# Kernel tuning notes

Hardware: AMD Instinct MI355X
Metric: run time of the kernel (lower is better)

Reference implementation:

```python
import jax, jax.numpy as jnp
import numpy as np

B, N, F = 1048576, 20, 7
RADIUS = 0.15
L1, L2 = 0.1, 2.0


def setup_inputs() -> dict:
    key = jax.random.key(0)
    ks = jax.random.split(key, 8)
    half = N // 2
    return {
        "x": jax.random.normal(ks[0], (B, N, F), dtype=jnp.float32),
        "W1": jax.random.normal(ks[1], (39, 64), dtype=jnp.float32) * 0.1,
        "b1": jax.random.normal(ks[2], (64,), dtype=jnp.float32) * 0.1,
        "W2": jax.random.normal(ks[3], (64, 64), dtype=jnp.float32) * 0.1,
        "b2": jax.random.normal(ks[4], (64,), dtype=jnp.float32) * 0.1,
        "W3": jax.random.normal(ks[5], (64, 5), dtype=jnp.float32) * 0.1,
        "b3": jax.random.normal(ks[6], (5,), dtype=jnp.float32) * 0.1,
        "idx": jax.random.randint(ks[7], (8,), 0, half, dtype=jnp.int32),
    }


def _build_observation(x, idx):
    # x: [B, N, 7]; agent_index = 0 (init kwarg)
    agent_index = 0
    half = N // 2
    Bsz = x.shape[0]
    pos = x[:, agent_index, 0:2]                      # [B,2]
    o_self = x[:, agent_index, 0:5]                   # [B,5]

    # three random agent neighbors: rel goal-like quantity, then a zero column
    xi = x[:, idx[0:3], :]                            # [B,3,7]
    rel = xi[..., 5:7] + xi[..., 0:2] - pos[:, None]  # [B,3,2]
    mid = jnp.concatenate(
        [rel, jnp.zeros((Bsz, 3, 1), dtype=x.dtype)], axis=2
    ).reshape(Bsz, 9)

    # five random obstacles (second half): distance-masked relative pos + features
    jdx = idx[3:8] + half
    xo = x[:, jdx, :]                                 # [B,5,7]
    d = xo[..., 0:2] - pos[:, None]                   # [B,5,2]
    dist = jnp.linalg.norm(d, axis=-1)                # [B,5]
    mask = (dist < RADIUS)[..., None]                 # [B,5,1]
    a = jnp.where(mask, d, 0.0)                       # [B,5,2]
    f = jnp.where(mask, xo[..., 2:5], 0.0)            # [B,5,3]
    obst = jnp.concatenate([a, f], axis=2).reshape(Bsz, 25)

    return jnp.concatenate([o_self, mid, obst], axis=1)  # [B,39]


def reference(x, W1, b1, W2, b2, W3, b3, idx):
    obs = _build_observation(x, idx)
    h = jax.nn.relu(obs @ W1 + b1)
    h = jax.nn.relu(h @ W2 + b2)
    r = h @ W3 + b3                                   # [B,5]
    res = jnp.stack([r[:, 1] - r[:, 2], r[:, 3] - r[:, 4]], axis=1) * L1
    res = jnp.where(jnp.abs(res) > 1.0, jnp.sign(res) * L2, res)
    return res
```

## Files before the change

### kernel.cpp

```cpp
#include <hip/hip_runtime.h>
#include <math.h>


#define NROW 20
#define NF   7
#define ITEM_F (NROW * NF)
#define BLOCK 256

typedef float v2 __attribute__((ext_vector_type(2)));

__device__ __forceinline__ void row_fma(v2 (&h)[32], float o,
                                        const float* __restrict__ wrow) {
    const v2* w = (const v2*)wrow;
    #pragma unroll
    for (int k = 0; k < 32; k++) {
        v2 ov; ov.x = o; ov.y = o;
        h[k] = __builtin_elementwise_fma(ov, w[k], h[k]);
    }
}

__global__ __launch_bounds__(BLOCK, 2) void maddpg_kernel(
    const float* __restrict__ x,
    const float* __restrict__ W1, const float* __restrict__ b1,
    const float* __restrict__ W2, const float* __restrict__ b2,
    const float* __restrict__ W3, const float* __restrict__ b3,
    const int*   __restrict__ idx,
    float2*      __restrict__ out,
    int nitems)
{
    const int tid = threadIdx.x;
    const long b  = (long)blockIdx.x * BLOCK + tid;
    if (b >= nitems) return;

    const float* xb = x + b * (long)ITEM_F;

    float4 s0 = *(const float4*)(xb);
    float  s4 = xb[4];
    const float px = s0.x, py = s0.y;

    float mo[6];
    #pragma unroll
    for (int t = 0; t < 3; t++) {
        const float* xr = xb + idx[t] * NF;
        float2 p01 = *(const float2*)(xr);
        float2 p56 = *(const float2*)(xr + 5);
        mo[2*t + 0] = p56.x + p01.x - px;
        mo[2*t + 1] = p56.y + p01.y - py;
    }

    float oa[5][5];
    int   anyt[5];
    #pragma unroll
    for (int t = 0; t < 5; t++) {
        const float* xr = xb + (idx[3 + t] + NROW/2) * NF;
        float4 q  = *(const float4*)(xr);
        float  q4 = xr[4];
        float dx = q.x - px, dy = q.y - py;
        bool  m  = sqrtf(dx*dx + dy*dy) < 0.15f;
        oa[t][0] = m ? dx  : 0.0f;
        oa[t][1] = m ? dy  : 0.0f;
        oa[t][2] = m ? q.z : 0.0f;
        oa[t][3] = m ? q.w : 0.0f;
        oa[t][4] = m ? q4  : 0.0f;
        anyt[t]  = __any(m);
    }

    v2 h[32];
    const v2* b1v = (const v2*)b1;
    #pragma unroll
    for (int k = 0; k < 32; k++) h[k] = b1v[k];

    row_fma(h, s0.x, W1 + 0*64);
    row_fma(h, s0.y, W1 + 1*64);
    row_fma(h, s0.z, W1 + 2*64);
    row_fma(h, s0.w, W1 + 3*64);
    row_fma(h, s4,   W1 + 4*64);
    #pragma unroll
    for (int t = 0; t < 3; t++) {
        row_fma(h, mo[2*t + 0], W1 + (5 + 3*t)*64);
        row_fma(h, mo[2*t + 1], W1 + (6 + 3*t)*64);
    }
    #pragma unroll
    for (int t = 0; t < 5; t++) {
        if (anyt[t]) {
            #pragma unroll
            for (int j = 0; j < 5; j++)
                row_fma(h, oa[t][j], W1 + (14 + 5*t + j)*64);
        }
    }

    v2 a[32];
    #pragma unroll
    for (int k = 0; k < 32; k++) {
        a[k].x = fmaxf(h[k].x, 0.0f);
        a[k].y = fmaxf(h[k].y, 0.0f);
    }

    const v2* b2v = (const v2*)b2;
    #pragma unroll
    for (int k = 0; k < 32; k++) h[k] = b2v[k];
    #pragma unroll
    for (int i = 0; i < 64; i++) {
        float o = (i & 1) ? a[i >> 1].y : a[i >> 1].x;
        row_fma(h, o, W2 + i*64);
    }
    #pragma unroll
    for (int k = 0; k < 32; k++) {
        a[k].x = fmaxf(h[k].x, 0.0f);
        a[k].y = fmaxf(h[k].y, 0.0f);
    }

    v2 rA; rA.x = b3[1]; rA.y = b3[2];
    v2 rB; rB.x = b3[3]; rB.y = b3[4];
    #pragma unroll
    for (int i = 0; i < 64; i++) {
        float o = (i & 1) ? a[i >> 1].y : a[i >> 1].x;
        const float* w = W3 + i*5;
        v2 ov; ov.x = o; ov.y = o;
        v2 wA; wA.x = w[1]; wA.y = w[2];
        v2 wB; wB.x = w[3]; wB.y = w[4];
        rA = __builtin_elementwise_fma(ov, wA, rA);
        rB = __builtin_elementwise_fma(ov, wB, rB);
    }

    float v0 = (rA.x - rA.y) * 0.1f;
    float v1 = (rB.x - rB.y) * 0.1f;
    if (fabsf(v0) > 1.0f) v0 = copysignf(2.0f, v0);
    if (fabsf(v1) > 1.0f) v1 = copysignf(2.0f, v1);

    out[b] = make_float2(v0, v1);
}

extern "C" void kernel_launch(void* const* d_in, const int* in_sizes, int n_in,
                              void* d_out, int out_size, void* d_ws, size_t ws_size,
                              hipStream_t stream) {
    const float* x  = (const float*)d_in[0];
    const float* W1 = (const float*)d_in[1];
    const float* b1 = (const float*)d_in[2];
    const float* W2 = (const float*)d_in[3];
    const float* b2 = (const float*)d_in[4];
    const float* W3 = (const float*)d_in[5];
    const float* b3 = (const float*)d_in[6];
    const int*   idx = (const int*)d_in[7];
    float2* out = (float2*)d_out;

    int nitems = in_sizes[0] / ITEM_F;
    int grid = (nitems + BLOCK - 1) / BLOCK;
    maddpg_kernel<<<grid, BLOCK, 0, stream>>>(x, W1, b1, W2, b2, W3, b3, idx,
                                              out, nitems);
}
```

Baseline: 935.0 us.

## Stage item rows through LDS with coalesced chunked loads

Replaces per-thread strided gathers of each item's 140 floats with block-cooperative coalesced loads of 56-float chunks (8 rows) into shared memory. The stages are software-pipelined so the next chunk's global load is in flight while the current one is extracted from LDS. It loads the full 140 floats per item (more bytes than the sparse gather) but with fully coalesced access, and adds about 59KB of LDS plus several barriers, which may limit occupancy.

Result: slower. 1.049 ms (+12.2%).

```diff
diff --git a/kernel.cpp b/kernel.cpp
--- a/kernel.cpp
+++ b/kernel.cpp
@@ -6,6 +6,8 @@
 #define NF   7
 #define ITEM_F (NROW * NF)
 #define BLOCK 256
+#define LSTF  58
+#define LSTF2 29
 
 typedef float v2 __attribute__((ext_vector_type(2)));
 
@@ -17,6 +19,53 @@
         v2 ov; ov.x = o; ov.y = o;
         h[k] = __builtin_elementwise_fma(ov, w[k], h[k]);
     }
+}
+
+template<int F2PI, bool CLAMP>
+__device__ __forceinline__ void stage_load(const float* __restrict__ gbase,
+                                           int tid, int ilim, v2 (&st)[F2PI]) {
+    constexpr int SI = 256 / F2PI;
+    constexpr int SV = 256 % F2PI;
+    int i = tid / F2PI;
+    int v = tid - i * F2PI;
+    #pragma unroll
+    for (int k = 0; k < F2PI; k++) {
+        int ic = CLAMP ? ((i < ilim) ? i : ilim) : i;
+        st[k] = *(const v2*)(gbase + (long)ic * ITEM_F + 2 * v);
+        i += SI; v += SV;
+        if (v >= F2PI) { v -= F2PI; i += 1; }
+    }
+}
+
+template<int F2PI>
+__device__ __forceinline__ void stage_write(float* __restrict__ ldsf,
+                                            int tid, const v2 (&st)[F2PI]) {
+    constexpr int SI = 256 / F2PI;
+    constexpr int SV = 256 % F2PI;
+    v2* lf2 = (v2*)ldsf;
+    int i = tid / F2PI;
+    int v = tid - i * F2PI;
+    #pragma unroll
+    for (int k = 0; k < F2PI; k++) {
+        lf2[i * LSTF2 + v] = st[k];
+        i += SI; v += SV;
+        if (v >= F2PI) { v -= F2PI; i += 1; }
+    }
+}
+
+__device__ __forceinline__ void obst_extract(const float* __restrict__ myl,
+                                             int base, float px, float py,
+                                             float (&o)[5], int& any) {
+    float q0 = myl[base + 0], q1 = myl[base + 1], q2 = myl[base + 2];
+    float q3 = myl[base + 3], q4 = myl[base + 4];
+    float dx = q0 - px, dy = q1 - py;
+    bool  m  = sqrtf(dx*dx + dy*dy) < 0.15f;
+    o[0] = m ? dx : 0.0f;
+    o[1] = m ? dy : 0.0f;
+    o[2] = m ? q2 : 0.0f;
+    o[3] = m ? q3 : 0.0f;
+    o[4] = m ? q4 : 0.0f;
+    any  = __any(m);
 }
 
 __global__ __launch_bounds__(BLOCK, 2) void maddpg_kernel(
@@ -28,41 +77,83 @@
     float2*      __restrict__ out,
     int nitems)
 {
-    const int tid = threadIdx.x;
-    const long b  = (long)blockIdx.x * BLOCK + tid;
-    if (b >= nitems) return;
-
-    const float* xb = x + b * (long)ITEM_F;
-
-    float4 s0 = *(const float4*)(xb);
-    float  s4 = xb[4];
-    const float px = s0.x, py = s0.y;
-
+    __shared__ float lds[BLOCK * LSTF];
+
+    const int  tid  = threadIdx.x;
+    const long blk0 = (long)blockIdx.x * BLOCK;
+    const float* xblk = x + blk0 * ITEM_F;
+
+    long rem  = (long)nitems - blk0;
+    const bool full = (rem >= BLOCK);
+    int  ilim = full ? (BLOCK - 1) : ((int)rem - 1);
+
+    int sidx[8];
+    #pragma unroll
+    for (int t = 0; t < 8; t++) sidx[t] = idx[t];
+
+    float px, py, s2v, s3v, s4v;
     float mo[6];
-    #pragma unroll
-    for (int t = 0; t < 3; t++) {
-        const float* xr = xb + idx[t] * NF;
-        float2 p01 = *(const float2*)(xr);
-        float2 p56 = *(const float2*)(xr + 5);
-        mo[2*t + 0] = p56.x + p01.x - px;
-        mo[2*t + 1] = p56.y + p01.y - py;
-    }
-
     float oa[5][5];
     int   anyt[5];
+
+    const float* myl = lds + tid * LSTF;
+
+    v2 st0[28];
+    if (full) stage_load<28, false>(xblk + 0 * 56, tid, ilim, st0);
+    else      stage_load<28, true >(xblk + 0 * 56, tid, ilim, st0);
+    stage_write<28>(lds, tid, st0);
+    __syncthreads();
+
+    v2 st1[28];
+    if (full) stage_load<28, false>(xblk + 1 * 56, tid, ilim, st1);
+    else      stage_load<28, true >(xblk + 1 * 56, tid, ilim, st1);
+
+    px = myl[0]; py = myl[1]; s2v = myl[2]; s3v = myl[3]; s4v = myl[4];
+    #pragma unroll
+    for (int t = 0; t < 3; t++) {
+        int r = sidx[t];
+        if ((r >> 3) == 0) {
+            int base = (r & 7) * NF;
+            float ax = myl[base + 0], ay = myl[base + 1];
+            float bx = myl[base + 5], by = myl[base + 6];
+            mo[2*t + 0] = bx + ax - px;
+            mo[2*t + 1] = by + ay - py;
+        }
+    }
+    __syncthreads();
+    stage_write<28>(lds, tid, st1);
+    __syncthreads();
+
+    v2 st2[14];
+    if (full) stage_load<14, false>(xblk + 2 * 56, tid, ilim, st2);
+    else      stage_load<14, true >(xblk + 2 * 56, tid, ilim, st2);
+
+    #pragma unroll
+    for (int t = 0; t < 3; t++) {
+        int r = sidx[t];
+        if ((r >> 3) == 1) {
+            int base = (r & 7) * NF;
+            float ax = myl[base + 0], ay = myl[base + 1];
+            float bx = myl[base + 5], by = myl[base + 6];
+            mo[2*t + 0] = bx + ax - px;
+            mo[2*t + 1] = by + ay - py;
+        }
+    }
     #pragma unroll
     for (int t = 0; t < 5; t++) {
-        const float* xr = xb + (idx[3 + t] + NROW/2) * NF;
-        float4 q  = *(const float4*)(xr);
-        float  q4 = xr[4];
-        float dx = q.x - px, dy = q.y - py;
-        bool  m  = sqrtf(dx*dx + dy*dy) < 0.15f;
-        oa[t][0] = m ? dx  : 0.0f;
-        oa[t][1] = m ? dy  : 0.0f;
-        oa[t][2] = m ? q.z : 0.0f;
-        oa[t][3] = m ? q.w : 0.0f;
-        oa[t][4] = m ? q4  : 0.0f;
-        anyt[t]  = __any(m);
+        int r = sidx[3 + t] + NROW/2;
+        if ((r >> 3) == 1)
+            obst_extract(myl, (r & 7) * NF, px, py, oa[t], anyt[t]);
+    }
+    __syncthreads();
+    stage_write<14>(lds, tid, st2);
+    __syncthreads();
+
+    #pragma unroll
+    for (int t = 0; t < 5; t++) {
+        int r = sidx[3 + t] + NROW/2;
+        if ((r >> 3) == 2)
+            obst_extract(myl, (r & 7) * NF, px, py, oa[t], anyt[t]);
     }
 
     v2 h[32];
@@ -70,11 +161,11 @@
     #pragma unroll
     for (int k = 0; k < 32; k++) h[k] = b1v[k];
 
-    row_fma(h, s0.x, W1 + 0*64);
-    row_fma(h, s0.y, W1 + 1*64);
-    row_fma(h, s0.z, W1 + 2*64);
-    row_fma(h, s0.w, W1 + 3*64);
-    row_fma(h, s4,   W1 + 4*64);
+    row_fma(h, px,  W1 + 0*64);
+    row_fma(h, py,  W1 + 1*64);
+    row_fma(h, s2v, W1 + 2*64);
+    row_fma(h, s3v, W1 + 3*64);
+    row_fma(h, s4v, W1 + 4*64);
     #pragma unroll
     for (int t = 0; t < 3; t++) {
         row_fma(h, mo[2*t + 0], W1 + (5 + 3*t)*64);
@@ -128,7 +219,8 @@
     if (fabsf(v0) > 1.0f) v0 = copysignf(2.0f, v0);
     if (fabsf(v1) > 1.0f) v1 = copysignf(2.0f, v1);
 
-    out[b] = make_float2(v0, v1);
+    if (blk0 + tid < (long)nitems)
+        out[blk0 + tid] = make_float2(v0, v1);
 }
 
 extern "C" void kernel_launch(void* const* d_in, const int* in_sizes, int n_in,
```
